# Kernel tuning notes

Hardware: AMD Instinct MI355X
Metric: run time of the kernel (lower is better)

Reference implementation:

```python
import jax, jax.numpy as jnp
import numpy as np

B, C, H, W = 4, 256, 64, 64
CR = max(C // 8, 1)  # reduced channels
EPS = 1e-12  # F.normalize eps


def setup_inputs() -> dict:
    key = jax.random.key(0)
    ks = jax.random.split(key, 8)
    s = 1.0 / np.sqrt(C)
    return {
        "x": jax.random.normal(ks[0], (B, C, H, W), dtype=jnp.float32),
        "Wq": jax.random.normal(ks[1], (CR, C), dtype=jnp.float32) * s,
        "bq": jax.random.normal(ks[2], (CR,), dtype=jnp.float32) * s,
        "Wk": jax.random.normal(ks[3], (CR, C), dtype=jnp.float32) * s,
        "bk": jax.random.normal(ks[4], (CR,), dtype=jnp.float32) * s,
        "Wv": jax.random.normal(ks[5], (C, C), dtype=jnp.float32) * s,
        "bv": jax.random.normal(ks[6], (C,), dtype=jnp.float32) * s,
        "gamma": jax.random.normal(ks[7], (1,), dtype=jnp.float32),
    }


def reference(x, Wq, bq, Wk, bk, Wv, bv, gamma):
    b, c, h, w = x.shape
    xf = x.reshape(b, c, h * w)  # [B, C, N]
    # 1x1 convs are per-pixel linear maps
    q = jnp.einsum("rc,bcn->brn", Wq, xf) + bq[None, :, None]  # [B, CR, N]
    k = jnp.einsum("rc,bcn->brn", Wk, xf) + bk[None, :, None]  # [B, CR, N]
    v = jnp.einsum("dc,bcn->bdn", Wv, xf) + bv[None, :, None]  # [B, C, N]
    # attention = bmm(key^T, query): [B, N, N]
    attn = jnp.einsum("brn,brm->bnm", k, q)
    attn = jax.nn.relu(attn)
    # L1 normalize along dim=1 (rows), matching F.normalize(p=1, dim=1)
    denom = jnp.maximum(jnp.sum(jnp.abs(attn), axis=1, keepdims=True), EPS)
    attn = attn / denom
    out = jnp.einsum("bcn,bnm->bcm", v, attn).reshape(b, c, h, w)
    return gamma[0] * out + x
```

## Files before the change

kernel.cpp:

```cpp
#include <hip/hip_runtime.h>
#include <hip/hip_bf16.h>

#define NB 4
#define NC 256
#define NN 4096
#define NCR 32
#define PITCH 72

typedef __attribute__((ext_vector_type(8))) short short8_t;
typedef __attribute__((ext_vector_type(4))) float f32x4;
typedef __attribute__((ext_vector_type(2))) int int2_t;
typedef __attribute__((ext_vector_type(4))) int int4_t;
typedef __attribute__((ext_vector_type(4))) float float4_t;

static __device__ __forceinline__ unsigned short f2bf(float f) {
  unsigned u = __builtin_bit_cast(unsigned, f);
  u += 0x7FFFu + ((u >> 16) & 1u);
  return (unsigned short)(u >> 16);
}

static __device__ __forceinline__ unsigned cvt_pk(float lo, float hi) {
  unsigned r;
  asm("v_cvt_pk_bf16_f32 %0, %1, %2" : "=v"(r) : "v"(lo), "v"(hi));
  return r;
}

__global__ __launch_bounds__(64) void pack_w_kernel(
    const float* __restrict__ Wq, const float* __restrict__ Wk,
    const float* __restrict__ Wv, unsigned short* __restrict__ Wbf)
{
  const int row = blockIdx.x;
  const int t = threadIdx.x;
  const float* src = row < 32 ? Wq + (size_t)row * NC
                   : (row < 64 ? Wk + (size_t)(row - 32) * NC
                               : Wv + (size_t)(row - 64) * NC);
  float4_t v = *(const float4_t*)(src + t * 4);
  int2_t p;
  p[0] = cvt_pk(v[0], v[1]);
  p[1] = cvt_pk(v[2], v[3]);
  *(int2_t*)(Wbf + (size_t)row * NC + t * 4) = p;
}

__global__ __launch_bounds__(256) void xpose_kernel(
    const float* __restrict__ x, unsigned short* __restrict__ xT)
{
  __shared__ float tile[32][65];
  const int bid = blockIdx.x;
  const int mt = bid & 63, kt = (bid >> 6) & 7, b = bid >> 9;
  const int m0 = mt * 64, k0 = kt * 32;
  const int tid = threadIdx.x;

  const float* xb = x + (size_t)b * NC * NN + (size_t)k0 * NN + m0;
#pragma unroll
  for (int p = 0; p < 8; p++) {
    const int r = p * 4 + (tid >> 6);
    tile[r][tid & 63] = xb[(size_t)r * NN + (tid & 63)];
  }
  __syncthreads();

  const int m = tid >> 2, kq = (tid & 3) * 8;
  int4_t o;
#pragma unroll
  for (int j = 0; j < 4; j++)
    o[j] = cvt_pk(tile[kq + 2 * j][m], tile[kq + 2 * j + 1][m]);
  *(int4_t*)(xT + ((size_t)b * NN + m0 + m) * NC + k0 + kq) = o;
}

__global__ __launch_bounds__(256, 2) void qkv_kernel(
    const unsigned short* __restrict__ xT, const unsigned short* __restrict__ Wbf,
    const float* __restrict__ bq, const float* __restrict__ bk,
    const float* __restrict__ bv,
    unsigned short* __restrict__ Qt, unsigned short* __restrict__ Kt,
    unsigned short* __restrict__ Vt)
{
  const int bid = blockIdx.x;
  const int b   = bid >> 7;
  const int m0  = (bid & 127) * 32;
  const int tid = threadIdx.x;
  const int w    = tid >> 6;
  const int lane = tid & 63;
  const int lg   = lane >> 4;
  const int lm   = lane & 15;

  const unsigned short* xrow0 = xT + ((size_t)b * NN + m0 + lm) * NC + lg * 8;
  const unsigned short* xrow1 = xrow0 + 16 * NC;
  const unsigned short* wrow  = Wbf + (size_t)(w * 80 + lm) * NC + lg * 8;

  const f32x4 zero4 = {0.f, 0.f, 0.f, 0.f};
  f32x4 acc[5][2];
#pragma unroll
  for (int df = 0; df < 5; df++)
#pragma unroll
    for (int mf = 0; mf < 2; mf++) acc[df][mf] = zero4;

#pragma unroll
  for (int kc = 0; kc < 8; kc++) {
    const short8_t xf0 = *(const short8_t*)(xrow0 + kc * 32);
    const short8_t xf1 = *(const short8_t*)(xrow1 + kc * 32);
#pragma unroll
    for (int df = 0; df < 5; df++) {
      const short8_t wf = *(const short8_t*)(wrow + (size_t)df * 16 * NC + kc * 32);
      acc[df][0] = __builtin_amdgcn_mfma_f32_16x16x32_bf16(xf0, wf, acc[df][0], 0, 0, 0);
      acc[df][1] = __builtin_amdgcn_mfma_f32_16x16x32_bf16(xf1, wf, acc[df][1], 0, 0, 0);
    }
  }

#pragma unroll
  for (int df = 0; df < 5; df++) {
    const int dbase = w * 80 + df * 16;
    if (dbase < 64) {
      const bool isq = dbase < 32;
      const float bia = isq ? bq[dbase + lm] : bk[dbase - 32 + lm];
      unsigned short* dst = isq ? Qt : Kt;
      const int dcol = (isq ? dbase : dbase - 32) + lm;
#pragma unroll
      for (int mf = 0; mf < 2; mf++)
#pragma unroll
        for (int i = 0; i < 4; i++) {
          const int m = m0 + mf * 16 + lg * 4 + i;
          dst[((size_t)b * NN + m) * NCR + dcol] = f2bf(acc[df][mf][i] + bia);
        }
    } else {
      const int c = dbase - 64 + lm;
      const float bia = bv[c];
#pragma unroll
      for (int mf = 0; mf < 2; mf++) {
        int2_t p;
        p[0] = cvt_pk(acc[df][mf][0] + bia, acc[df][mf][1] + bia);
        p[1] = cvt_pk(acc[df][mf][2] + bia, acc[df][mf][3] + bia);
        *(int2_t*)(Vt + ((size_t)b * NC + c) * NN + m0 + mf * 16 + lg * 4) = p;
      }
    }
  }
}

__global__ __launch_bounds__(256, 2) void attn_kernel(
    const unsigned short* __restrict__ Qt, const unsigned short* __restrict__ Kt,
    const unsigned short* __restrict__ Vt, const float* __restrict__ x,
    const float* __restrict__ gamma, float* __restrict__ out)
{
  __shared__ unsigned short Slds[2][64 * PITCH];
  __shared__ float dlds[4][64];

  const int bid = blockIdx.x;
  const int xcd = bid & 7;
  const int b   = xcd >> 1;
  const int ch  = xcd & 1;
  const int m0  = (bid >> 3) * 64;
  const int tid = threadIdx.x;
  const int w    = tid >> 6;
  const int lane = tid & 63;
  const int lg   = lane >> 4;
  const int lm   = lane & 15;

  const unsigned short* Qb = Qt + (size_t)b * NN * NCR;
  const unsigned short* Kp = Kt + (size_t)b * NN * NCR +
                             (size_t)(w * 16 + lm) * NCR + lg * 8;
  const unsigned short* pV[2];
#pragma unroll
  for (int cf = 0; cf < 2; cf++)
    pV[cf] = Vt + ((size_t)b * NC + ch * 128 + w * 32 + cf * 16 + lm) * NN + lg * 8;

  short8_t qf[4];
#pragma unroll
  for (int mf = 0; mf < 4; mf++)
    qf[mf] = *(const short8_t*)(Qb + (size_t)(m0 + mf * 16 + lm) * NCR + lg * 8);

  const f32x4 zero4 = {0.f, 0.f, 0.f, 0.f};
  f32x4 acc[2][4];
#pragma unroll
  for (int cf = 0; cf < 2; cf++)
#pragma unroll
    for (int mf = 0; mf < 4; mf++) acc[cf][mf] = zero4;
  float dsum[4] = {0.f, 0.f, 0.f, 0.f};

  short8_t kA, kB;
  kA = *(const short8_t*)(Kp);

  const int swofs = w * 16 + lg * 4;

#define AITER(T, KC, KN, BUF) {                                               \
    const int ncur = (T) * 64;                                                \
       \
    short8_t vc[2][2];                                                        \
    _Pragma("unroll") for (int cf = 0; cf < 2; cf++) {                        \
      vc[cf][0] = *(const short8_t*)(pV[cf] + ncur);                          \
      vc[cf][1] = *(const short8_t*)(pV[cf] + ncur + 32);                     \
    }                                                                         \
    const int n1 = (((T) + 1) & 63) * 64;                                     \
    KN = *(const short8_t*)(Kp + (size_t)n1 * NCR);                           \
    _Pragma("unroll") for (int mf = 0; mf < 4; mf++) {                        \
      f32x4 s = __builtin_amdgcn_mfma_f32_16x16x32_bf16(KC, qf[mf], zero4, 0, 0, 0); \
      float s0 = fmaxf(s[0], 0.f), s1 = fmaxf(s[1], 0.f);                     \
      float s2 = fmaxf(s[2], 0.f), s3 = fmaxf(s[3], 0.f);                     \
      dsum[mf] += (s0 + s1) + (s2 + s3);                                      \
      int2_t p; p[0] = cvt_pk(s0, s1); p[1] = cvt_pk(s2, s3);                 \
      *(int2_t*)(&Slds[BUF][(mf * 16 + lm) * PITCH + swofs]) = p;             \
    }                                                                         \
    __syncthreads();                                                          \
    __builtin_amdgcn_s_setprio(1);                                            \
    _Pragma("unroll") for (int nch = 0; nch < 2; nch++) {                     \
      short8_t sf[4];                                                         \
      _Pragma("unroll") for (int mf = 0; mf < 4; mf++)                        \
        sf[mf] = *(const short8_t*)(&Slds[BUF][(mf * 16 + lm) * PITCH +       \
                                              nch * 32 + lg * 8]);            \
      _Pragma("unroll") for (int cf = 0; cf < 2; cf++)                        \
        _Pragma("unroll") for (int mf = 0; mf < 4; mf++)                      \
          acc[cf][mf] = __builtin_amdgcn_mfma_f32_16x16x32_bf16(              \
              vc[cf][nch], sf[mf], acc[cf][mf], 0, 0, 0);                     \
    }                                                                         \
    __builtin_amdgcn_s_setprio(0);                                            \
  }

#pragma unroll 1
  for (int t = 0; t < 64; t += 2) {
    AITER(t, kA, kB, 0)
    AITER(t + 1, kB, kA, 1)
  }
#undef AITER

#pragma unroll
  for (int mf = 0; mf < 4; mf++) {
    float v = dsum[mf];
    v += __shfl_xor(v, 16);
    v += __shfl_xor(v, 32);
    if (lane < 16) dlds[w][mf * 16 + lane] = v;
  }
  __syncthreads();

  const float g0 = gamma[0];
  float rden[4];
#pragma unroll
  for (int mf = 0; mf < 4; mf++) {
    const int mloc = mf * 16 + lm;
    float den = dlds[0][mloc] + dlds[1][mloc] + dlds[2][mloc] + dlds[3][mloc];
    den = den > 1e-12f ? den : 1e-12f;
    rden[mf] = 1.0f / den;
  }

  const float* xb = x + (size_t)b * NC * NN;
  float* ob = out + (size_t)b * NC * NN;
#pragma unroll
  for (int cf = 0; cf < 2; cf++) {
#pragma unroll
    for (int i = 0; i < 4; i++) {
      const int c = ch * 128 + w * 32 + cf * 16 + lg * 4 + i;
#pragma unroll
      for (int mf = 0; mf < 4; mf++) {
        const int m = m0 + mf * 16 + lm;
        ob[(size_t)c * NN + m] = g0 * acc[cf][mf][i] * rden[mf] + xb[(size_t)c * NN + m];
      }
    }
  }
}

extern "C" void kernel_launch(void* const* d_in, const int* in_sizes, int n_in,
                              void* d_out, int out_size, void* d_ws, size_t ws_size,
                              hipStream_t stream) {
  const float* x     = (const float*)d_in[0];
  const float* Wq    = (const float*)d_in[1];
  const float* bq    = (const float*)d_in[2];
  const float* Wk    = (const float*)d_in[3];
  const float* bk    = (const float*)d_in[4];
  const float* Wv    = (const float*)d_in[5];
  const float* bv    = (const float*)d_in[6];
  const float* gamma = (const float*)d_in[7];
  float* out = (float*)d_out;

  unsigned short* Wbf = (unsigned short*)d_ws;
  unsigned short* xT  = Wbf + (size_t)320 * NC;
  unsigned short* Qt  = xT + (size_t)NB * NN * NC;
  unsigned short* Kt  = Qt + (size_t)NB * NN * NCR;
  unsigned short* Vt  = Kt + (size_t)NB * NN * NCR;

  hipLaunchKernelGGL(pack_w_kernel, dim3(320), dim3(64), 0, stream,
                     Wq, Wk, Wv, Wbf);
  hipLaunchKernelGGL(xpose_kernel, dim3(2048), dim3(256), 0, stream, x, xT);
  hipLaunchKernelGGL(qkv_kernel, dim3(512), dim3(256), 0, stream,
                     xT, Wbf, bq, bk, bv, Qt, Kt, Vt);
  hipLaunchKernelGGL(attn_kernel, dim3(512), dim3(256), 0, stream,
                     Qt, Kt, Vt, x, gamma, out);
}
```

Baseline: 102.3 us.

## Keep attention scores in registers via 32x32 MFMA and permlane swap, dropping LDS

```diff
diff --git a/kernel.cpp b/kernel.cpp
--- a/kernel.cpp
+++ b/kernel.cpp
@@ -5,10 +5,10 @@
 #define NC 256
 #define NN 4096
 #define NCR 32
-#define PITCH 72
 
 typedef __attribute__((ext_vector_type(8))) short short8_t;
 typedef __attribute__((ext_vector_type(4))) float f32x4;
+typedef __attribute__((ext_vector_type(16))) float f32x16;
 typedef __attribute__((ext_vector_type(2))) int int2_t;
 typedef __attribute__((ext_vector_type(4))) int int4_t;
 typedef __attribute__((ext_vector_type(4))) float float4_t;
@@ -139,118 +139,99 @@
     const unsigned short* __restrict__ Vt, const float* __restrict__ x,
     const float* __restrict__ gamma, float* __restrict__ out)
 {
-  __shared__ unsigned short Slds[2][64 * PITCH];
-  __shared__ float dlds[4][64];
-
   const int bid = blockIdx.x;
   const int xcd = bid & 7;
+  const int idx = bid >> 3;
   const int b   = xcd >> 1;
-  const int ch  = xcd & 1;
-  const int m0  = (bid >> 3) * 64;
+  const int cr  = (xcd & 1) * 2 + (idx & 1);
+  const int mt  = idx >> 1;
   const int tid = threadIdx.x;
   const int w    = tid >> 6;
   const int lane = tid & 63;
-  const int lg   = lane >> 4;
-  const int lm   = lane & 15;
+  const int l31  = lane & 31;
+  const int h    = lane >> 5;
+
+  const int m0    = mt * 128 + w * 32;
+  const int cbase = cr * 64;
 
   const unsigned short* Qb = Qt + (size_t)b * NN * NCR;
-  const unsigned short* Kp = Kt + (size_t)b * NN * NCR +
-                             (size_t)(w * 16 + lm) * NCR + lg * 8;
-  const unsigned short* pV[2];
-#pragma unroll
-  for (int cf = 0; cf < 2; cf++)
-    pV[cf] = Vt + ((size_t)b * NC + ch * 128 + w * 32 + cf * 16 + lm) * NN + lg * 8;
-
-  short8_t qf[4];
-#pragma unroll
-  for (int mf = 0; mf < 4; mf++)
-    qf[mf] = *(const short8_t*)(Qb + (size_t)(m0 + mf * 16 + lm) * NCR + lg * 8);
-
-  const f32x4 zero4 = {0.f, 0.f, 0.f, 0.f};
-  f32x4 acc[2][4];
-#pragma unroll
-  for (int cf = 0; cf < 2; cf++)
-#pragma unroll
-    for (int mf = 0; mf < 4; mf++) acc[cf][mf] = zero4;
-  float dsum[4] = {0.f, 0.f, 0.f, 0.f};
-
-  short8_t kA, kB;
-  kA = *(const short8_t*)(Kp);
-
-  const int swofs = w * 16 + lg * 4;
-
-#define AITER(T, KC, KN, BUF) {                                               \
-    const int ncur = (T) * 64;                                                \
-       \
-    short8_t vc[2][2];                                                        \
-    _Pragma("unroll") for (int cf = 0; cf < 2; cf++) {                        \
-      vc[cf][0] = *(const short8_t*)(pV[cf] + ncur);                          \
-      vc[cf][1] = *(const short8_t*)(pV[cf] + ncur + 32);                     \
-    }                                                                         \
-    const int n1 = (((T) + 1) & 63) * 64;                                     \
-    KN = *(const short8_t*)(Kp + (size_t)n1 * NCR);                           \
-    _Pragma("unroll") for (int mf = 0; mf < 4; mf++) {                        \
-      f32x4 s = __builtin_amdgcn_mfma_f32_16x16x32_bf16(KC, qf[mf], zero4, 0, 0, 0); \
-      float s0 = fmaxf(s[0], 0.f), s1 = fmaxf(s[1], 0.f);                     \
-      float s2 = fmaxf(s[2], 0.f), s3 = fmaxf(s[3], 0.f);                     \
-      dsum[mf] += (s0 + s1) + (s2 + s3);                                      \
-      int2_t p; p[0] = cvt_pk(s0, s1); p[1] = cvt_pk(s2, s3);                 \
-      *(int2_t*)(&Slds[BUF][(mf * 16 + lm) * PITCH + swofs]) = p;             \
-    }                                                                         \
-    __syncthreads();                                                          \
+  const unsigned short* Kp = Kt + (size_t)b * NN * NCR + (size_t)l31 * NCR + h * 8;
+  const unsigned short* Vp0 = Vt + ((size_t)b * NC + cbase + l31) * NN + h * 8;
+  const unsigned short* Vp1 = Vp0 + (size_t)32 * NN;
+
+  const short8_t qf0 = *(const short8_t*)(Qb + (size_t)(m0 + l31) * NCR + h * 8);
+  const short8_t qf1 = *(const short8_t*)(Qb + (size_t)(m0 + l31) * NCR + 16 + h * 8);
+
+  f32x16 accA, accB, zero16;
+#pragma unroll
+  for (int i = 0; i < 16; i++) { accA[i] = 0.f; accB[i] = 0.f; zero16[i] = 0.f; }
+  float dsum = 0.f;
+
+  short8_t kA[2], kB[2], vA[2][2], vB[2][2];
+  kA[0] = *(const short8_t*)(Kp);
+  kA[1] = *(const short8_t*)(Kp + 16);
+  vA[0][0] = *(const short8_t*)(Vp0);
+  vA[0][1] = *(const short8_t*)(Vp0 + 16);
+  vA[1][0] = *(const short8_t*)(Vp1);
+  vA[1][1] = *(const short8_t*)(Vp1 + 16);
+
+#define AITER(T, KC, KN, VC, VN) {                                            \
+    const int n1 = (((T) + 1) & 127) * 32;                                    \
+    KN[0] = *(const short8_t*)(Kp + (size_t)n1 * NCR);                        \
+    KN[1] = *(const short8_t*)(Kp + (size_t)n1 * NCR + 16);                   \
+    VN[0][0] = *(const short8_t*)(Vp0 + n1);                                  \
+    VN[0][1] = *(const short8_t*)(Vp0 + n1 + 16);                             \
+    VN[1][0] = *(const short8_t*)(Vp1 + n1);                                  \
+    VN[1][1] = *(const short8_t*)(Vp1 + n1 + 16);                             \
+                        \
+    f32x16 s = __builtin_amdgcn_mfma_f32_32x32x16_bf16(KC[0], qf0, zero16, 0, 0, 0); \
+    s = __builtin_amdgcn_mfma_f32_32x32x16_bf16(KC[1], qf1, s, 0, 0, 0);      \
+    float r_[16];                                                             \
+    _Pragma("unroll") for (int i = 0; i < 16; i++) r_[i] = fmaxf(s[i], 0.f);  \
+    dsum += (((r_[0] + r_[1]) + (r_[2] + r_[3])) +                            \
+             ((r_[4] + r_[5]) + (r_[6] + r_[7]))) +                           \
+            (((r_[8] + r_[9]) + (r_[10] + r_[11])) +                          \
+             ((r_[12] + r_[13]) + (r_[14] + r_[15])));                        \
+    unsigned p0 = cvt_pk(r_[0], r_[1]), p1 = cvt_pk(r_[2], r_[3]);            \
+    unsigned p2 = cvt_pk(r_[4], r_[5]), p3 = cvt_pk(r_[6], r_[7]);            \
+    unsigned p4 = cvt_pk(r_[8], r_[9]), p5 = cvt_pk(r_[10], r_[11]);          \
+    unsigned p6 = cvt_pk(r_[12], r_[13]), p7 = cvt_pk(r_[14], r_[15]);        \
+    asm("v_permlane32_swap_b32 %0, %1" : "+v"(p0), "+v"(p2));                 \
+    asm("v_permlane32_swap_b32 %0, %1" : "+v"(p1), "+v"(p3));                 \
+    asm("v_permlane32_swap_b32 %0, %1" : "+v"(p4), "+v"(p6));                 \
+    asm("v_permlane32_swap_b32 %0, %1" : "+v"(p5), "+v"(p7));                 \
+    int4_t pb0i = {(int)p0, (int)p1, (int)p2, (int)p3};                       \
+    int4_t pb1i = {(int)p4, (int)p5, (int)p6, (int)p7};                       \
+    const short8_t pb0 = __builtin_bit_cast(short8_t, pb0i);                  \
+    const short8_t pb1 = __builtin_bit_cast(short8_t, pb1i);                  \
     __builtin_amdgcn_s_setprio(1);                                            \
-    _Pragma("unroll") for (int nch = 0; nch < 2; nch++) {                     \
-      short8_t sf[4];                                                         \
-      _Pragma("unroll") for (int mf = 0; mf < 4; mf++)                        \
-        sf[mf] = *(const short8_t*)(&Slds[BUF][(mf * 16 + lm) * PITCH +       \
-                                              nch * 32 + lg * 8]);            \
-      _Pragma("unroll") for (int cf = 0; cf < 2; cf++)                        \
-        _Pragma("unroll") for (int mf = 0; mf < 4; mf++)                      \
-          acc[cf][mf] = __builtin_amdgcn_mfma_f32_16x16x32_bf16(              \
-              vc[cf][nch], sf[mf], acc[cf][mf], 0, 0, 0);                     \
-    }                                                                         \
+    accA = __builtin_amdgcn_mfma_f32_32x32x16_bf16(VC[0][0], pb0, accA, 0, 0, 0); \
+    accA = __builtin_amdgcn_mfma_f32_32x32x16_bf16(VC[0][1], pb1, accA, 0, 0, 0); \
+    accB = __builtin_amdgcn_mfma_f32_32x32x16_bf16(VC[1][0], pb0, accB, 0, 0, 0); \
+    accB = __builtin_amdgcn_mfma_f32_32x32x16_bf16(VC[1][1], pb1, accB, 0, 0, 0); \
     __builtin_amdgcn_s_setprio(0);                                            \
   }
 
 #pragma unroll 1
-  for (int t = 0; t < 64; t += 2) {
-    AITER(t, kA, kB, 0)
-    AITER(t + 1, kB, kA, 1)
+  for (int t = 0; t < 128; t += 2) {
+    AITER(t, kA, kB, vA, vB)
+    AITER(t + 1, kB, kA, vB, vA)
   }
 #undef AITER
 
-#pragma unroll
-  for (int mf = 0; mf < 4; mf++) {
-    float v = dsum[mf];
-    v += __shfl_xor(v, 16);
-    v += __shfl_xor(v, 32);
-    if (lane < 16) dlds[w][mf * 16 + lane] = v;
-  }
-  __syncthreads();
-
+  dsum += __shfl_xor(dsum, 32);
+  const float rden = 1.0f / (dsum > 1e-12f ? dsum : 1e-12f);
   const float g0 = gamma[0];
-  float rden[4];
-#pragma unroll
-  for (int mf = 0; mf < 4; mf++) {
-    const int mloc = mf * 16 + lm;
-    float den = dlds[0][mloc] + dlds[1][mloc] + dlds[2][mloc] + dlds[3][mloc];
-    den = den > 1e-12f ? den : 1e-12f;
-    rden[mf] = 1.0f / den;
-  }
-
-  const float* xb = x + (size_t)b * NC * NN;
-  float* ob = out + (size_t)b * NC * NN;
-#pragma unroll
-  for (int cf = 0; cf < 2; cf++) {
-#pragma unroll
-    for (int i = 0; i < 4; i++) {
-      const int c = ch * 128 + w * 32 + cf * 16 + lg * 4 + i;
-#pragma unroll
-      for (int mf = 0; mf < 4; mf++) {
-        const int m = m0 + mf * 16 + lm;
-        ob[(size_t)c * NN + m] = g0 * acc[cf][mf][i] * rden[mf] + xb[(size_t)c * NN + m];
-      }
-    }
+
+  const int m = m0 + l31;
+  const float* xb = x + (size_t)b * NC * NN + m;
+  float* ob = out + (size_t)b * NC * NN + m;
+#pragma unroll
+  for (int r = 0; r < 16; r++) {
+    const int c0 = cbase + (r & 3) + 8 * (r >> 2) + 4 * h;
+    ob[(size_t)c0 * NN] = g0 * accA[r] * rden + xb[(size_t)c0 * NN];
+    const int c1 = c0 + 32;
+    ob[(size_t)c1 * NN] = g0 * accB[r] * rden + xb[(size_t)c1 * NN];
   }
 }
 
```

Result: slower. 177.2 us (+73.2%).
